# Optimization experiments

Hardware: AMD Instinct MI355X
Metric: run time of the kernel (lower is better)

## Reference

```python
import jax, jax.numpy as jnp
import numpy as np

N, C, H, W = 32, 512, 56, 56
L, CT, HEAD, GROUPS = 64, 512, 16, 16
SIZE, POS_DIM = 14, 49  # PosEncoder(size=14, num_downsample=1) -> 14^2 // 4 = 49


def setup_inputs() -> dict:
    key = jax.random.key(0)
    ks = jax.random.split(key, 8)
    return {
        "feature": jax.random.normal(ks[0], (N, C, H, W), jnp.float32),
        "w_tc": jax.random.normal(ks[1], (L, C), jnp.float32) * 0.02,
        "b_tc": jnp.zeros((L,), jnp.float32),
        "w_val": jax.random.normal(ks[2], (GROUPS, CT // GROUPS, C // GROUPS), jnp.float32) * 0.02,
        "b_val": jnp.zeros((CT,), jnp.float32),
        "w_ds3": jax.random.normal(ks[3], (1, 1, 3, 3), jnp.float32) * 0.1,
        "b_ds3": jnp.zeros((1,), jnp.float32),
        "w_ds1": jax.random.normal(ks[4], (1, 1), jnp.float32) * 0.1,
        "b_ds1": jnp.zeros((1,), jnp.float32),
        "w_pos": jax.random.normal(ks[5], (POS_DIM, POS_DIM), jnp.float32) * 0.02,
        "b_pos": jnp.zeros((POS_DIM,), jnp.float32),
        "w_tok": jax.random.normal(ks[6], (CT, CT + POS_DIM), jnp.float32) * 0.02,
        "b_tok": jnp.zeros((CT,), jnp.float32),
    }


def reference(feature, w_tc, b_tc, w_val, b_val, w_ds3, b_ds3, w_ds1, b_ds1,
              w_pos, b_pos, w_tok, b_tok):
    n, c, h, w = feature.shape
    hw = h * w
    # --- static token coefficients: 1x1 conv C->L, scale, softmax over HW ---
    tc = jnp.einsum('nchw,lc->nlhw', feature, w_tc) + b_tc[None, :, None, None]
    tc = tc.reshape(n, 1, L, hw).transpose(0, 1, 3, 2) / np.sqrt(c)  # (N,1,HW,L)
    tc = jax.nn.softmax(tc, axis=2)
    # --- grouped 1x1 conv value: C -> CT (groups=16) ---
    fg = feature.reshape(n, GROUPS, c // GROUPS, hw)
    val = jnp.einsum('ngci,gdc->ngdi', fg, w_val).reshape(n, CT, hw) + b_val[None, :, None]
    val = val.reshape(n, HEAD, CT // HEAD, hw)
    # --- token aggregation: (N,h,CT/h,HW) @ (N,1,HW,L) -> (N,CT,L) ---
    tokens = jnp.matmul(val, tc).reshape(n, CT, -1)
    # --- PosEncoder: view coef maps as images, nearest-resize to 14x14 ---
    pc = tc.reshape(n * L, 1, h, w)  # torch .view memory reinterpretation
    ih = (jnp.arange(SIZE) * h) // SIZE
    iw = (jnp.arange(SIZE) * w) // SIZE
    pc = pc[:, :, ih][:, :, :, iw]  # (N*L,1,14,14) nearest interpolate
    # conv3x3 stride 2 pad 1: 14 -> 7
    pc = jax.lax.conv_general_dilated(pc, w_ds3, (2, 2), ((1, 1), (1, 1))) + b_ds3[None, :, None, None]
    # conv1x1 (1->1)
    pc = jnp.einsum('nchw,dc->ndhw', pc, w_ds1) + b_ds1[None, :, None, None]
    pc = pc.reshape(n, L, POS_DIM).transpose(0, 2, 1)  # (N,49,L)
    pos = jnp.einsum('ncl,dc->ndl', pc, w_pos) + b_pos[None, :, None]
    # --- concat + final 1x1 conv1d (CT+49 -> CT) ---
    tokens = jnp.concatenate([tokens, pos], axis=1)
    tokens = jnp.einsum('ncl,dc->ndl', tokens, w_tok) + b_tok[None, :, None]
    return tokens  # (N, CT, L)
```

## Files before the change

### kernel.cpp

```cpp
#include <hip/hip_runtime.h>
#include <hip/hip_bf16.h>
#include <cstddef>
#include <cstdint>

namespace {

constexpr int kN = 32;
constexpr int kC = 512;
constexpr int kHW = 3136;
constexpr int kL = 64;
constexpr int kCT = 512;
constexpr int kTok = 561;
constexpr int kKcat = 576;

typedef float fx4 __attribute__((ext_vector_type(4)));
typedef float f32x4 __attribute__((ext_vector_type(4)));
typedef short short8 __attribute__((ext_vector_type(8)));
typedef unsigned int u32x2 __attribute__((ext_vector_type(2)));

static __device__ inline unsigned short bf16_1(float x) {
  __hip_bfloat16 h = __float2bfloat16(x);
  unsigned short u;
  __builtin_memcpy(&u, &h, 2);
  return u;
}
static __device__ inline unsigned pk2(float a, float b) {
  __hip_bfloat162 h2 = __float22bfloat162_rn(make_float2(a, b));
  unsigned u;
  __builtin_memcpy(&u, &h2, 4);
  return u;
}
static __device__ inline float bf2f(unsigned short h) {
  unsigned u = (unsigned)h << 16;
  float f;
  __builtin_memcpy(&f, &u, 4);
  return f;
}

__global__ __launch_bounds__(256) void prep_kernel(
    const float* __restrict__ w_tok, const float* __restrict__ w_val,
    const float* __restrict__ b_val, const float* __restrict__ b_tok,
    const float* __restrict__ w_tc, unsigned short* __restrict__ wcat16,
    float* __restrict__ cst, unsigned short* __restrict__ wtc16,
    float* __restrict__ denom, unsigned short* __restrict__ bcat16) {
  int idx = blockIdx.x * 256 + threadIdx.x;
  if (idx < kCT * kKcat) {
    int d = idx / kKcat;
    int c = idx - d * kKcat;
    float v = 0.f;
    if (c < kCT) {
      int g = c >> 5, k = c & 31;
      const float* wt = w_tok + (size_t)d * kTok + g * 32;
      const float* wv = w_val + g * 1024 + k;
      float s = 0.f;
#pragma unroll
      for (int dp = 0; dp < 32; ++dp) s += wt[dp] * wv[dp * 32];
      v = s;
    } else if (c < kTok) {
      v = w_tok[(size_t)d * kTok + c];
    }
    wcat16[idx] = bf16_1(v);
    return;
  }
  idx -= kCT * kKcat;
  if (idx < kCT) {
    float s = b_tok[idx];
    for (int c = 0; c < kCT; ++c) s += w_tok[(size_t)idx * kTok + c] * b_val[c];
    cst[idx] = s;
    return;
  }
  idx -= kCT;
  if (idx < kL * kC) {
    wtc16[idx] = bf16_1(w_tc[idx]);
    return;
  }
  idx -= kL * kC;
  if (idx < kN * kL) {
    denom[idx] = 0.f;
    return;
  }
  idx -= kN * kL;
  if (idx < kN * kL * 15) {
    int n = idx / (kL * 15);
    int r = idx - n * (kL * 15);
    int l = r / 15;
    int k = kTok + (r - l * 15);
    bcat16[(size_t)n * kL * kKcat + (size_t)l * kKcat + k] = 0;
  }
}

__global__ __launch_bounds__(256) void tc_gemm2_kernel(
    const float* __restrict__ feat, const unsigned short* __restrict__ wtc16,
    const float* __restrict__ b_tc, unsigned short* __restrict__ expT,
    float* __restrict__ denom) {
  const int n = blockIdx.y;
  const int pb = blockIdx.x * 256;
  const int tid = threadIdx.x;
  const int wave = tid >> 6, lane = tid & 63;
  const int quad = lane >> 4, l16 = lane & 15;
  __shared__ unsigned short Bs[256][72];
  __shared__ float bsm[64];
  __shared__ float denom_s[64];
  if (tid < 64) {
    bsm[tid] = b_tc[tid];
    denom_s[tid] = 0.f;
  }

  f32x4 acc[4][4];
#pragma unroll
  for (int i = 0; i < 4; ++i)
#pragma unroll
    for (int j = 0; j < 4; ++j) acc[i][j] = (f32x4){0.f, 0.f, 0.f, 0.f};

  const float* fb = feat + (size_t)n * kC * kHW;
  const int bc4 = (tid & 15) * 4, bpl0 = (tid >> 4) * 4;
  int pe_[4];
#pragma unroll
  for (int pass = 0; pass < 4; ++pass) {
    int pe = pb + bpl0 + pass * 64;
    pe_[pass] = pe < 3132 ? pe : 3132;
  }

  fx4 va[4][4], vb[4][4];
  auto LOADT = [&](int c0, fx4 (&v)[4][4]) {
#pragma unroll
    for (int pass = 0; pass < 4; ++pass) {
      const float* s = fb + (size_t)(c0 + bc4) * kHW + pe_[pass];
#pragma unroll
      for (int r = 0; r < 4; ++r) v[pass][r] = *(const fx4*)(s + (size_t)r * kHW);
    }
  };
  auto STORET = [&](fx4 (&v)[4][4]) {
#pragma unroll
    for (int pass = 0; pass < 4; ++pass) {
      int pl = bpl0 + pass * 4 * 16;
      (void)pl;
      int base = bpl0 + pass * 64;
#pragma unroll
      for (int j = 0; j < 4; ++j) {
        u32x2 w = {pk2(v[pass][0][j], v[pass][1][j]),
                   pk2(v[pass][2][j], v[pass][3][j])};
        *(u32x2*)&Bs[base + j][bc4] = w;
      }
    }
  };
  auto COMPUTE = [&](int c0) {
#pragma unroll
    for (int ks = 0; ks < 2; ++ks) {
      short8 a[4], b[4];
#pragma unroll
      for (int i = 0; i < 4; ++i)
        a[i] = *(const short8*)(wtc16 + (size_t)(i * 16 + l16) * kC + c0 +
                                ks * 32 + quad * 8);
#pragma unroll
      for (int j = 0; j < 4; ++j)
        b[j] = *(const short8*)&Bs[wave * 64 + j * 16 + l16][ks * 32 + quad * 8];
#pragma unroll
      for (int i = 0; i < 4; ++i)
#pragma unroll
        for (int j = 0; j < 4; ++j)
          acc[i][j] = __builtin_amdgcn_mfma_f32_16x16x32_bf16(a[i], b[j],
                                                              acc[i][j], 0, 0, 0);
    }
  };

  LOADT(0, va);
#pragma unroll
  for (int c0 = 0; c0 < kC; c0 += 128) {
    STORET(va);
    __syncthreads();
    LOADT(c0 + 64, vb);
    COMPUTE(c0);
    __syncthreads();
    STORET(vb);
    __syncthreads();
    if (c0 + 128 < kC) LOADT(c0 + 128, va);
    COMPUTE(c0 + 64);
    __syncthreads();
  }

  const float inv = 0.04419417382415922f;
  unsigned short* eb = expT + (size_t)n * kL * kHW;
  float dsum[4][4];
#pragma unroll
  for (int ti = 0; ti < 4; ++ti)
#pragma unroll
    for (int r = 0; r < 4; ++r) dsum[ti][r] = 0.f;

#pragma unroll
  for (int ti = 0; ti < 4; ++ti) {
#pragma unroll
    for (int tj = 0; tj < 4; ++tj) {
      int pg = pb + wave * 64 + tj * 16 + l16;
      bool ok = pg < kHW;
#pragma unroll
      for (int r = 0; r < 4; ++r) {
        int l = ti * 16 + quad * 4 + r;
        float e = 0.f;
        if (ok) {
          float raw = (acc[ti][tj][r] + bsm[l]) * inv;
          unsigned short h = bf16_1(__expf(raw));
          eb[(size_t)l * kHW + pg] = h;
          e = bf2f(h);
        }
        dsum[ti][r] += e;
      }
    }
  }
#pragma unroll
  for (int off = 1; off < 16; off <<= 1) {
#pragma unroll
    for (int ti = 0; ti < 4; ++ti)
#pragma unroll
      for (int r = 0; r < 4; ++r) dsum[ti][r] += __shfl_xor(dsum[ti][r], off);
  }
  if (l16 == 0) {
#pragma unroll
    for (int ti = 0; ti < 4; ++ti)
#pragma unroll
      for (int r = 0; r < 4; ++r)
        atomicAdd(&denom_s[ti * 16 + quad * 4 + r], dsum[ti][r]);
  }
  __syncthreads();
  if (tid < 64) atomicAdd(&denom[n * 64 + tid], denom_s[tid]);
}

__global__ __launch_bounds__(256) void m_gemm2_kernel(
    const float* __restrict__ feat, const unsigned short* __restrict__ expT,
    float* __restrict__ part, int klen) {
  const int cb = blockIdx.x * 256;
  const int n = blockIdx.y;
  const int s = blockIdx.z;
  const int p0s = s * klen;
  const int tid = threadIdx.x;
  const int wave = tid >> 6, lane = tid & 63;
  const int quad = lane >> 4, l16 = lane & 15;
  __shared__ unsigned short Bs[256][72];

  f32x4 acc[4][4];
#pragma unroll
  for (int i = 0; i < 4; ++i)
#pragma unroll
    for (int j = 0; j < 4; ++j) acc[i][j] = (f32x4){0.f, 0.f, 0.f, 0.f};

  const float* fb = feat + (size_t)n * kC * kHW;
  const unsigned short* ebase = expT + (size_t)n * kL * kHW;
  const int bkg = (tid >> 6) * 16, bcr = tid & 63;

  fx4 va[4][4], vb[4][4];
  auto LOADT = [&](int p0, fx4 (&v)[4][4]) {
#pragma unroll
    for (int pass = 0; pass < 4; ++pass) {
      const float* src = fb + (size_t)(cb + pass * 64 + bcr) * kHW + p0 + bkg;
#pragma unroll
      for (int u = 0; u < 4; ++u) v[pass][u] = *(const fx4*)(src + u * 4);
    }
  };
  auto STORET = [&](fx4 (&v)[4][4]) {
#pragma unroll
    for (int pass = 0; pass < 4; ++pass) {
#pragma unroll
      for (int u = 0; u < 4; ++u) {
        u32x2 w = {pk2(v[pass][u][0], v[pass][u][1]),
                   pk2(v[pass][u][2], v[pass][u][3])};
        *(u32x2*)&Bs[pass * 64 + bcr][bkg + u * 4] = w;
      }
    }
  };
  auto COMPUTE = [&](int p0) {
#pragma unroll
    for (int ks = 0; ks < 2; ++ks) {
      short8 a[4], b[4];
#pragma unroll
      for (int i = 0; i < 4; ++i)
        a[i] = *(const short8*)(ebase + (size_t)(i * 16 + l16) * kHW + p0 +
                                ks * 32 + quad * 8);
#pragma unroll
      for (int j = 0; j < 4; ++j)
        b[j] = *(const short8*)&Bs[wave * 64 + j * 16 + l16][ks * 32 + quad * 8];
#pragma unroll
      for (int i = 0; i < 4; ++i)
#pragma unroll
        for (int j = 0; j < 4; ++j)
          acc[i][j] = __builtin_amdgcn_mfma_f32_16x16x32_bf16(a[i], b[j],
                                                              acc[i][j], 0, 0, 0);
    }
  };

  const int nk = klen >> 6;
  LOADT(p0s, va);
  for (int t = 0; t < nk; t += 2) {
    const int p0 = p0s + t * 64;
    STORET(va);
    __syncthreads();
    const bool more1 = (t + 1) < nk;
    if (more1) LOADT(p0 + 64, vb);
    COMPUTE(p0);
    __syncthreads();
    if (more1) {
      STORET(vb);
      __syncthreads();
      if (t + 2 < nk) LOADT(p0 + 128, va);
      COMPUTE(p0 + 64);
      __syncthreads();
    }
  }

  float* ob = part + (size_t)(s * kN + n) * kL * kCT;
#pragma unroll
  for (int ti = 0; ti < 4; ++ti) {
#pragma unroll
    for (int tj = 0; tj < 4; ++tj) {
      int cg = cb + wave * 64 + tj * 16 + l16;
#pragma unroll
      for (int r = 0; r < 4; ++r) {
        int l = ti * 16 + quad * 4 + r;
        ob[(size_t)l * kCT + cg] = acc[ti][tj][r];
      }
    }
  }
}

__global__ __launch_bounds__(256) void reduce_pos_kernel(
    const float* __restrict__ part, const float* __restrict__ denom,
    unsigned short* __restrict__ bcat16, const unsigned short* __restrict__ expT,
    const float* __restrict__ w3, const float* __restrict__ b3,
    const float* __restrict__ w1, const float* __restrict__ b1,
    float* __restrict__ pcl, int ksplit) {
  int idx = blockIdx.x * 256 + threadIdx.x;
  if (idx < kN * kL * kCT) {
    int n = idx >> 15;
    int r = idx & 32767;
    int l = r >> 9;
    int c = r & 511;
    float s = 0.f;
    for (int ss = 0; ss < ksplit; ++ss)
      s += part[(size_t)ss * (kN * kL * kCT) + idx];
    float si = 1.f / denom[n * 64 + l];
    bcat16[(size_t)n * kL * kKcat + (size_t)l * kKcat + c] = bf16_1(s * si);
    return;
  }
  idx -= kN * kL * kCT;
  if (idx >= kN * kL * 49) return;
  int n = idx / (kL * 49);
  int r = idx - n * (kL * 49);
  int lp = r / 49;
  int o = r - lp * 49;
  int y = o / 7, x = o - y * 7;
  const unsigned short* eb = expT + (size_t)n * kL * kHW;
  const float* dB = denom + n * 64;
  float a = 0.f;
#pragma unroll
  for (int dy = 0; dy < 3; ++dy) {
    int i = 2 * y - 1 + dy;
    if (i < 0 || i >= 14) continue;
#pragma unroll
    for (int dx = 0; dx < 3; ++dx) {
      int j = 2 * x - 1 + dx;
      if (j < 0 || j >= 14) continue;
      int t = 224 * i + 4 * j;
      int lsm = t & 63;
      int p = lp * 49 + (t >> 6);
      float e = bf2f(eb[(size_t)lsm * kHW + p]);
      a += w3[dy * 3 + dx] * (e / dB[lsm]);
    }
  }
  pcl[(size_t)n * kL * 49 + lp * 49 + o] = (a + b3[0]) * w1[0] + b1[0];
}

__global__ __launch_bounds__(256) void pos_out2_kernel(
    const float* __restrict__ pcl, const float* __restrict__ wp,
    const float* __restrict__ bp, unsigned short* __restrict__ bcat16) {
  const int n = blockIdx.x;
  __shared__ float t[64 * 49];
  for (int i = threadIdx.x; i < 64 * 49; i += 256)
    t[i] = pcl[(size_t)n * 64 * 49 + i];
  __syncthreads();
  for (int o = threadIdx.x; o < 64 * 49; o += 256) {
    int l = o / 49, d = o - l * 49;
    float s = bp[d];
#pragma unroll 7
    for (int q = 0; q < 49; ++q) s += wp[d * 49 + q] * t[l * 49 + q];
    bcat16[(size_t)n * kL * kKcat + (size_t)l * kKcat + kCT + d] = bf16_1(s);
  }
}

__global__ __launch_bounds__(256) void out_gemm2_kernel(
    const unsigned short* __restrict__ wcat16,
    const unsigned short* __restrict__ bcat16, const float* __restrict__ cst,
    float* __restrict__ out) {
  const int db = blockIdx.x * 64;
  const int n = blockIdx.y;
  const int tid = threadIdx.x;
  const int wave = tid >> 6, lane = tid & 63;
  const int quad = lane >> 4, l16 = lane & 15;
  __shared__ float csm[64];
  if (tid < 64) csm[tid] = cst[db + tid];
  __syncthreads();

  f32x4 acc[4];
#pragma unroll
  for (int j = 0; j < 4; ++j) acc[j] = (f32x4){0.f, 0.f, 0.f, 0.f};

  const unsigned short* ab = wcat16 + (size_t)(db + wave * 16 + l16) * kKcat;
  const unsigned short* bb = bcat16 + (size_t)n * kL * kKcat;
#pragma unroll
  for (int k0 = 0; k0 < kKcat; k0 += 32) {
    short8 a = *(const short8*)(ab + k0 + quad * 8);
    short8 b[4];
#pragma unroll
    for (int j = 0; j < 4; ++j)
      b[j] = *(const short8*)(bb + (size_t)(j * 16 + l16) * kKcat + k0 + quad * 8);
#pragma unroll
    for (int j = 0; j < 4; ++j)
      acc[j] = __builtin_amdgcn_mfma_f32_16x16x32_bf16(a, b[j], acc[j], 0, 0, 0);
  }

  float* ob = out + (size_t)n * kCT * kL;
#pragma unroll
  for (int tj = 0; tj < 4; ++tj) {
    int lg = tj * 16 + l16;
#pragma unroll
    for (int r = 0; r < 4; ++r) {
      int dl = wave * 16 + quad * 4 + r;
      ob[(size_t)(db + dl) * kL + lg] = acc[tj][r] + csm[dl];
    }
  }
}

}

extern "C" void kernel_launch(void* const* d_in, const int* in_sizes, int n_in,
                              void* d_out, int out_size, void* d_ws,
                              size_t ws_size, hipStream_t stream) {
  (void)in_sizes; (void)n_in; (void)out_size;
  const float* feat  = (const float*)d_in[0];
  const float* w_tc  = (const float*)d_in[1];
  const float* b_tc  = (const float*)d_in[2];
  const float* w_val = (const float*)d_in[3];
  const float* b_val = (const float*)d_in[4];
  const float* w_ds3 = (const float*)d_in[5];
  const float* b_ds3 = (const float*)d_in[6];
  const float* w_ds1 = (const float*)d_in[7];
  const float* b_ds1 = (const float*)d_in[8];
  const float* w_pos = (const float*)d_in[9];
  const float* b_pos = (const float*)d_in[10];
  const float* w_tok = (const float*)d_in[11];
  const float* b_tok = (const float*)d_in[12];
  float* out = (float*)d_out;

  float* ws = (float*)d_ws;
  size_t off = 0;
  unsigned short* expT = (unsigned short*)(ws + off);   off += (size_t)kN * kL * kHW / 2;
  unsigned short* bcat16 = (unsigned short*)(ws + off); off += (size_t)kN * kL * kKcat / 2;
  unsigned short* wcat16 = (unsigned short*)(ws + off); off += (size_t)kCT * kKcat / 2;
  unsigned short* wtc16 = (unsigned short*)(ws + off);  off += (size_t)kL * kC / 2;
  float* cst = ws + off;   off += kCT;
  float* denom = ws + off; off += kN * kL;
  float* pcl = ws + off;   off += (size_t)kN * kL * 49;
  float* part = ws + off;

  int ksplit = 7;
  if (ws_size < (off + (size_t)7 * kN * kL * kCT) * sizeof(float)) ksplit = 1;
  const int klen = kHW / ksplit;

  prep_kernel<<<1410, 256, 0, stream>>>(w_tok, w_val, b_val, b_tok, w_tc,
                                        wcat16, cst, wtc16, denom, bcat16);
  tc_gemm2_kernel<<<dim3(13, kN), 256, 0, stream>>>(feat, wtc16, b_tc, expT,
                                                    denom);
  m_gemm2_kernel<<<dim3(2, kN, ksplit), 256, 0, stream>>>(feat, expT, part,
                                                          klen);
  reduce_pos_kernel<<<4488, 256, 0, stream>>>(part, denom, bcat16, expT, w_ds3,
                                              b_ds3, w_ds1, b_ds1, pcl, ksplit);
  pos_out2_kernel<<<kN, 256, 0, stream>>>(pcl, w_pos, b_pos, bcat16);
  out_gemm2_kernel<<<dim3(8, kN), 256, 0, stream>>>(wcat16, bcat16, cst, out);
}
```

Measured before the change: 436.1 us.

## Emit bf16 feature copy in tc GEMM and stream it directly into aggregation GEMM

The coefficient GEMM now also writes a bf16 copy of the feature map while it already has it loaded. The aggregation GEMM reads that copy straight into MFMA operands, dropping its own fp32 load, conversion and LDS staging. The tc GEMM pixel tile is halved to 128 so more blocks launch, and the K-split rises to 14 when workspace allows. This adds a large bf16 write, extra workspace, and more partial sums for the reduction kernel. Total DRAM traffic stays about the same unless the bf16 copy is served from the large last-level cache.

```diff
diff --git a/kernel.cpp b/kernel.cpp
--- a/kernel.cpp
+++ b/kernel.cpp
@@ -92,13 +92,13 @@
 __global__ __launch_bounds__(256) void tc_gemm2_kernel(
     const float* __restrict__ feat, const unsigned short* __restrict__ wtc16,
     const float* __restrict__ b_tc, unsigned short* __restrict__ expT,
-    float* __restrict__ denom) {
+    unsigned short* __restrict__ feat16, float* __restrict__ denom) {
   const int n = blockIdx.y;
-  const int pb = blockIdx.x * 256;
+  const int pb = blockIdx.x * 128;
   const int tid = threadIdx.x;
   const int wave = tid >> 6, lane = tid & 63;
   const int quad = lane >> 4, l16 = lane & 15;
-  __shared__ unsigned short Bs[256][72];
+  __shared__ unsigned short Bs[128][72];
   __shared__ float bsm[64];
   __shared__ float denom_s[64];
   if (tid < 64) {
@@ -106,35 +106,34 @@
     denom_s[tid] = 0.f;
   }
 
-  f32x4 acc[4][4];
+  f32x4 acc[4][2];
 #pragma unroll
   for (int i = 0; i < 4; ++i)
 #pragma unroll
-    for (int j = 0; j < 4; ++j) acc[i][j] = (f32x4){0.f, 0.f, 0.f, 0.f};
+    for (int j = 0; j < 2; ++j) acc[i][j] = (f32x4){0.f, 0.f, 0.f, 0.f};
 
   const float* fb = feat + (size_t)n * kC * kHW;
+  unsigned short* f16b = feat16 + (size_t)n * kC * kHW;
   const int bc4 = (tid & 15) * 4, bpl0 = (tid >> 4) * 4;
-  int pe_[4];
-#pragma unroll
-  for (int pass = 0; pass < 4; ++pass) {
+  int pe_[2];
+#pragma unroll
+  for (int pass = 0; pass < 2; ++pass) {
     int pe = pb + bpl0 + pass * 64;
     pe_[pass] = pe < 3132 ? pe : 3132;
   }
 
-  fx4 va[4][4], vb[4][4];
-  auto LOADT = [&](int c0, fx4 (&v)[4][4]) {
-#pragma unroll
-    for (int pass = 0; pass < 4; ++pass) {
+  fx4 va[2][4], vb[2][4];
+  auto LOADT = [&](int c0, fx4 (&v)[2][4]) {
+#pragma unroll
+    for (int pass = 0; pass < 2; ++pass) {
       const float* s = fb + (size_t)(c0 + bc4) * kHW + pe_[pass];
 #pragma unroll
       for (int r = 0; r < 4; ++r) v[pass][r] = *(const fx4*)(s + (size_t)r * kHW);
     }
   };
-  auto STORET = [&](fx4 (&v)[4][4]) {
-#pragma unroll
-    for (int pass = 0; pass < 4; ++pass) {
-      int pl = bpl0 + pass * 4 * 16;
-      (void)pl;
+  auto STORET = [&](int c0, fx4 (&v)[2][4]) {
+#pragma unroll
+    for (int pass = 0; pass < 2; ++pass) {
       int base = bpl0 + pass * 64;
 #pragma unroll
       for (int j = 0; j < 4; ++j) {
@@ -142,23 +141,29 @@
                    pk2(v[pass][2][j], v[pass][3][j])};
         *(u32x2*)&Bs[base + j][bc4] = w;
       }
+#pragma unroll
+      for (int r = 0; r < 4; ++r) {
+        u32x2 wf = {pk2(v[pass][r][0], v[pass][r][1]),
+                    pk2(v[pass][r][2], v[pass][r][3])};
+        *(u32x2*)(f16b + (size_t)(c0 + bc4 + r) * kHW + pe_[pass]) = wf;
+      }
     }
   };
   auto COMPUTE = [&](int c0) {
 #pragma unroll
     for (int ks = 0; ks < 2; ++ks) {
-      short8 a[4], b[4];
+      short8 a[4], b[2];
 #pragma unroll
       for (int i = 0; i < 4; ++i)
         a[i] = *(const short8*)(wtc16 + (size_t)(i * 16 + l16) * kC + c0 +
                                 ks * 32 + quad * 8);
 #pragma unroll
-      for (int j = 0; j < 4; ++j)
-        b[j] = *(const short8*)&Bs[wave * 64 + j * 16 + l16][ks * 32 + quad * 8];
+      for (int j = 0; j < 2; ++j)
+        b[j] = *(const short8*)&Bs[wave * 32 + j * 16 + l16][ks * 32 + quad * 8];
 #pragma unroll
       for (int i = 0; i < 4; ++i)
 #pragma unroll
-        for (int j = 0; j < 4; ++j)
+        for (int j = 0; j < 2; ++j)
           acc[i][j] = __builtin_amdgcn_mfma_f32_16x16x32_bf16(a[i], b[j],
                                                               acc[i][j], 0, 0, 0);
     }
@@ -167,12 +172,12 @@
   LOADT(0, va);
 #pragma unroll
   for (int c0 = 0; c0 < kC; c0 += 128) {
-    STORET(va);
+    STORET(c0, va);
     __syncthreads();
     LOADT(c0 + 64, vb);
     COMPUTE(c0);
     __syncthreads();
-    STORET(vb);
+    STORET(c0 + 64, vb);
     __syncthreads();
     if (c0 + 128 < kC) LOADT(c0 + 128, va);
     COMPUTE(c0 + 64);
@@ -190,8 +195,8 @@
 #pragma unroll
   for (int ti = 0; ti < 4; ++ti) {
 #pragma unroll
-    for (int tj = 0; tj < 4; ++tj) {
-      int pg = pb + wave * 64 + tj * 16 + l16;
+    for (int tj = 0; tj < 2; ++tj) {
+      int pg = pb + wave * 32 + tj * 16 + l16;
       bool ok = pg < kHW;
 #pragma unroll
       for (int r = 0; r < 4; ++r) {
@@ -225,9 +230,10 @@
   if (tid < 64) atomicAdd(&denom[n * 64 + tid], denom_s[tid]);
 }
 
-__global__ __launch_bounds__(256) void m_gemm2_kernel(
-    const float* __restrict__ feat, const unsigned short* __restrict__ expT,
-    float* __restrict__ part, int klen) {
+__global__ __launch_bounds__(256) void m_gemm3_kernel(
+    const unsigned short* __restrict__ expT,
+    const unsigned short* __restrict__ feat16, float* __restrict__ part,
+    int klen) {
   const int cb = blockIdx.x * 256;
   const int n = blockIdx.y;
   const int s = blockIdx.z;
@@ -235,7 +241,6 @@
   const int tid = threadIdx.x;
   const int wave = tid >> 6, lane = tid & 63;
   const int quad = lane >> 4, l16 = lane & 15;
-  __shared__ unsigned short Bs[256][72];
 
   f32x4 acc[4][4];
 #pragma unroll
@@ -243,66 +248,40 @@
 #pragma unroll
     for (int j = 0; j < 4; ++j) acc[i][j] = (f32x4){0.f, 0.f, 0.f, 0.f};
 
-  const float* fb = feat + (size_t)n * kC * kHW;
-  const unsigned short* ebase = expT + (size_t)n * kL * kHW;
-  const int bkg = (tid >> 6) * 16, bcr = tid & 63;
-
-  fx4 va[4][4], vb[4][4];
-  auto LOADT = [&](int p0, fx4 (&v)[4][4]) {
-#pragma unroll
-    for (int pass = 0; pass < 4; ++pass) {
-      const float* src = fb + (size_t)(cb + pass * 64 + bcr) * kHW + p0 + bkg;
-#pragma unroll
-      for (int u = 0; u < 4; ++u) v[pass][u] = *(const fx4*)(src + u * 4);
-    }
+  const unsigned short* ea =
+      expT + (size_t)n * kL * kHW + (size_t)l16 * kHW + quad * 8;
+  const unsigned short* fbb =
+      feat16 + (size_t)n * kC * kHW +
+      (size_t)(cb + wave * 64 + l16) * kHW + quad * 8;
+
+  auto LOAD = [&](int p0, short8 (&a)[4], short8 (&b)[4]) {
+#pragma unroll
+    for (int i = 0; i < 4; ++i)
+      a[i] = *(const short8*)(ea + (size_t)i * 16 * kHW + p0);
+#pragma unroll
+    for (int j = 0; j < 4; ++j)
+      b[j] = *(const short8*)(fbb + (size_t)j * 16 * kHW + p0);
   };
-  auto STORET = [&](fx4 (&v)[4][4]) {
-#pragma unroll
-    for (int pass = 0; pass < 4; ++pass) {
-#pragma unroll
-      for (int u = 0; u < 4; ++u) {
-        u32x2 w = {pk2(v[pass][u][0], v[pass][u][1]),
-                   pk2(v[pass][u][2], v[pass][u][3])};
-        *(u32x2*)&Bs[pass * 64 + bcr][bkg + u * 4] = w;
-      }
-    }
+  auto MF = [&](short8 (&a)[4], short8 (&b)[4]) {
+#pragma unroll
+    for (int i = 0; i < 4; ++i)
+#pragma unroll
+      for (int j = 0; j < 4; ++j)
+        acc[i][j] =
+            __builtin_amdgcn_mfma_f32_16x16x32_bf16(a[i], b[j], acc[i][j], 0, 0, 0);
   };
-  auto COMPUTE = [&](int p0) {
-#pragma unroll
-    for (int ks = 0; ks < 2; ++ks) {
-      short8 a[4], b[4];
-#pragma unroll
-      for (int i = 0; i < 4; ++i)
-        a[i] = *(const short8*)(ebase + (size_t)(i * 16 + l16) * kHW + p0 +
-                                ks * 32 + quad * 8);
-#pragma unroll
-      for (int j = 0; j < 4; ++j)
-        b[j] = *(const short8*)&Bs[wave * 64 + j * 16 + l16][ks * 32 + quad * 8];
-#pragma unroll
-      for (int i = 0; i < 4; ++i)
-#pragma unroll
-        for (int j = 0; j < 4; ++j)
-          acc[i][j] = __builtin_amdgcn_mfma_f32_16x16x32_bf16(a[i], b[j],
-                                                              acc[i][j], 0, 0, 0);
-    }
-  };
-
-  const int nk = klen >> 6;
-  LOADT(p0s, va);
+
+  short8 aA[4], bA[4], aB[4], bB[4];
+  const int nk = klen >> 5;
+  LOAD(p0s, aA, bA);
   for (int t = 0; t < nk; t += 2) {
-    const int p0 = p0s + t * 64;
-    STORET(va);
-    __syncthreads();
-    const bool more1 = (t + 1) < nk;
-    if (more1) LOADT(p0 + 64, vb);
-    COMPUTE(p0);
-    __syncthreads();
-    if (more1) {
-      STORET(vb);
-      __syncthreads();
-      if (t + 2 < nk) LOADT(p0 + 128, va);
-      COMPUTE(p0 + 64);
-      __syncthreads();
+    const int p0 = p0s + t * 32;
+    const bool m1 = (t + 1) < nk;
+    if (m1) LOAD(p0 + 32, aB, bB);
+    MF(aA, bA);
+    if (m1) {
+      if (t + 2 < nk) LOAD(p0 + 64, aA, bA);
+      MF(aB, bB);
     }
   }
 
@@ -458,17 +437,19 @@
   float* cst = ws + off;   off += kCT;
   float* denom = ws + off; off += kN * kL;
   float* pcl = ws + off;   off += (size_t)kN * kL * 49;
+  unsigned short* feat16 = (unsigned short*)(ws + off); off += (size_t)kN * kC * kHW / 2;
   float* part = ws + off;
 
-  int ksplit = 7;
+  int ksplit = 14;
+  if (ws_size < (off + (size_t)14 * kN * kL * kCT) * sizeof(float)) ksplit = 7;
   if (ws_size < (off + (size_t)7 * kN * kL * kCT) * sizeof(float)) ksplit = 1;
   const int klen = kHW / ksplit;
 
   prep_kernel<<<1410, 256, 0, stream>>>(w_tok, w_val, b_val, b_tok, w_tc,
                                         wcat16, cst, wtc16, denom, bcat16);
-  tc_gemm2_kernel<<<dim3(13, kN), 256, 0, stream>>>(feat, wtc16, b_tc, expT,
-                                                    denom);
-  m_gemm2_kernel<<<dim3(2, kN, ksplit), 256, 0, stream>>>(feat, expT, part,
+  tc_gemm2_kernel<<<dim3(25, kN), 256, 0, stream>>>(feat, wtc16, b_tc, expT,
+                                                    feat16, denom);
+  m_gemm3_kernel<<<dim3(2, kN, ksplit), 256, 0, stream>>>(expT, feat16, part,
                                                           klen);
   reduce_pos_kernel<<<4488, 256, 0, stream>>>(part, denom, bcat16, expT, w_ds3,
                                               b_ds3, w_ds1, b_ds1, pcl, ksplit);
```

New measurement: 468.6 us. +7.5%, slower.
